# Kernel optimization log

Measured on AMD Instinct MI355X. Metric: run time of the kernel, lower is better.

Reference implementation:

```python
import jax, jax.numpy as jnp
import numpy as np

NUM_SRC = 100000  # block src nodes
NUM_DST = 50000   # block dst nodes (first NUM_DST of src in DGL convention)
E = 800000        # edges, avg in-degree 16
D = 128           # in_dim == out_dim


def setup_inputs() -> dict:
    key = jax.random.key(0)
    k0, k1, k2, k3, k4 = jax.random.split(key, 5)
    h = jax.random.normal(k0, (NUM_SRC, D), dtype=jnp.float32)
    src = jax.random.randint(k1, (E,), 0, NUM_SRC)
    dst = jax.random.randint(k2, (E,), 0, NUM_DST)
    # GraphConv params: weight (in_dim, out_dim), bias (out_dim,)
    W = jax.random.normal(k3, (D, D), dtype=jnp.float32) / np.float32(np.sqrt(D))
    b = jnp.zeros((D,), dtype=jnp.float32)
    # gene_attn: Linear(out_dim, 1, bias=False)
    w_attn = jax.random.normal(k4, (D, 1), dtype=jnp.float32) / np.float32(np.sqrt(D))
    return {"h": h, "src": src, "dst": dst, "W": W, "b": b, "w_attn": w_attn}


def reference(h, src, dst, W, b, w_attn):
    ones = jnp.ones(src.shape, dtype=h.dtype)
    # DGL GraphConv norm='both': scale by out-degree(src)^-1/2 and in-degree(dst)^-1/2,
    # degrees clamped to min 1 (allow_zero_in_degree=True).
    deg_src = jax.ops.segment_sum(ones, src, num_segments=NUM_SRC)
    deg_dst = jax.ops.segment_sum(ones, dst, num_segments=NUM_DST)
    h_src = h * jax.lax.rsqrt(jnp.maximum(deg_src, 1.0))[:, None]
    # gather neighbor feats [E, D] then scatter-sum into dst nodes
    agg = jax.ops.segment_sum(h_src[src], dst, num_segments=NUM_DST)
    agg = agg * jax.lax.rsqrt(jnp.maximum(deg_dst, 1.0))[:, None]
    # in_dim == out_dim -> aggregate-then-weight (DGL order)
    out = agg @ W + b  # h[:num_dst] equivalent: agg is already dst-sized
    alpha = jax.nn.sigmoid(out @ w_attn)  # [NUM_DST, 1]
    return out * alpha, alpha
```

## Files before the change

### kernel.cpp

```cpp
#include <hip/hip_runtime.h>
#include <hip/hip_bf16.h>
#include <math.h>

#define DD 128
#define MAXDEG 64
#define BKT 64
#define NB_MAX 1024
#define P_CH 8192
#define HBINS 16384
#define HBLK  32
#define HTHR  1024

using bf16x8 = __attribute__((ext_vector_type(8))) short;
using f32x4  = __attribute__((ext_vector_type(4))) float;

struct alignas(16) bfq { __hip_bfloat162 q[4]; };

__device__ inline float bf2f(short s) {
    unsigned int u = ((unsigned int)(unsigned short)s) << 16;
    float f;
    __builtin_memcpy(&f, &u, 4);
    return f;
}

__global__ __launch_bounds__(1024) void k1_kernel(
        const int* __restrict__ src, const int* __restrict__ dst,
        unsigned int* __restrict__ parts, unsigned int* __restrict__ bucket_cnt,
        int E, int NB, int nHist) {
    __shared__ unsigned int smem[HBINS];
    int t = threadIdx.x;
    int bid = blockIdx.x;
    if (bid < nHist) {
        int pass = bid / HBLK;
        int blk  = bid % HBLK;
        int lo   = pass * HBINS;
        for (int i = t; i < HBINS; i += 1024) smem[i] = 0;
        __syncthreads();
        int chunk = (E + HBLK - 1) / HBLK;
        int c0 = blk * chunk;
        int c1 = c0 + chunk; if (c1 > E) c1 = E;
        for (int i = c0 + t; i < c1; i += 1024) {
            unsigned int u = (unsigned int)(src[i] - lo);
            if (u < HBINS) atomicAdd(&smem[u], 1u);
        }
        __syncthreads();
        unsigned int* dstp = parts + ((size_t)bid << 14);
        for (int i = t; i < HBINS; i += 1024) dstp[i] = smem[i];
    } else {
        int b2 = bid - nHist;
        for (int b = t; b < NB; b += 1024) smem[b] = 0;
        __syncthreads();
        int c0 = b2 * P_CH;
        int c1 = c0 + P_CH; if (c1 > E) c1 = E;
        for (int i = c0 + t; i < c1; i += 1024)
            atomicAdd(&smem[dst[i] >> 6], 1u);
        __syncthreads();
        for (int b = t; b < NB; b += 1024)
            if (smem[b]) atomicAdd(&bucket_cnt[b], smem[b]);
    }
}

__global__ __launch_bounds__(256) void k2_kernel(
        const unsigned int* __restrict__ parts, unsigned int* __restrict__ deg_src,
        int num_src, const unsigned int* __restrict__ bucket_cnt,
        unsigned int* __restrict__ bucket_base, unsigned int* __restrict__ bucket_cur,
        int NB, int nMerge) {
    int bid = blockIdx.x;
    if (bid < nMerge) {
        int g = bid * 256 + threadIdx.x;
        if (g >= num_src) return;
        int pass = g >> 14;
        int r = g & (HBINS - 1);
        const unsigned int* p = parts + ((size_t)(pass * HBLK) << 14) + r;
        unsigned int s = 0;
#pragma unroll
        for (int b = 0; b < HBLK; ++b) s += p[(size_t)b << 14];
        deg_src[g] = s;
    } else {
        int lane = threadIdx.x;
        if (lane >= 64) return;
        unsigned int carry = 0;
        for (int b0 = 0; b0 < NB; b0 += 64) {
            int i = b0 + lane;
            unsigned int v = (i < NB) ? bucket_cnt[i] : 0u;
            unsigned int incl = v;
#pragma unroll
            for (int off = 1; off < 64; off <<= 1) {
                unsigned int u = __shfl_up(incl, off);
                if (lane >= off) incl += u;
            }
            unsigned int excl = incl - v + carry;
            if (i < NB) { bucket_base[i] = excl; bucket_cur[i] = excl; }
            carry += __shfl(incl, 63);
        }
        if (lane == 0) bucket_base[NB] = carry;
    }
}

__global__ __launch_bounds__(1024) void k3_kernel(
        const float* __restrict__ h, const unsigned int* __restrict__ deg_src,
        __hip_bfloat16* __restrict__ hb, const float* __restrict__ Wm,
        __hip_bfloat16* __restrict__ Wt, const int* __restrict__ src,
        const int* __restrict__ dst, unsigned int* __restrict__ bucket_cur,
        unsigned int* __restrict__ eparts, int E, int NB, int num_src,
        int nConv, int nWt) {
    __shared__ unsigned int smem[15360];
    int t = threadIdx.x;
    int bid = blockIdx.x;
    if (bid < nConv) {
        int idx = bid * 1024 + t;
        int total = num_src * (DD / 8);
        if (idx >= total) return;
        int row = idx >> 4;
        int c0  = (idx & 15) * 8;
        float nrm = rsqrtf(fmaxf((float)deg_src[row], 1.0f));
        const float4* p = reinterpret_cast<const float4*>(h + (size_t)row * DD + c0);
        float4 a = p[0], b = p[1];
        bfq o;
        o.q[0] = __float22bfloat162_rn(make_float2(a.x * nrm, a.y * nrm));
        o.q[1] = __float22bfloat162_rn(make_float2(a.z * nrm, a.w * nrm));
        o.q[2] = __float22bfloat162_rn(make_float2(b.x * nrm, b.y * nrm));
        o.q[3] = __float22bfloat162_rn(make_float2(b.z * nrm, b.w * nrm));
        *reinterpret_cast<bfq*>(hb + (size_t)row * DD + c0) = o;
    } else if (bid < nConv + nWt) {
        int idx = (bid - nConv) * 1024 + t;
        if (idx < DD * DD) {
            int c = idx >> 7, k = idx & 127;
            Wt[idx] = __float2bfloat16(Wm[k * DD + c]);
        }
    } else {
        int b2 = bid - nConv - nWt;
        unsigned int*   stage_s = smem;
        unsigned short* stage_d = (unsigned short*)(smem + 8192);
        unsigned int*   lhist   = smem + 12288;
        unsigned int*   lbase   = smem + 13312;
        unsigned int*   gbase   = smem + 14336;
        for (int b = t; b < NB_MAX; b += 1024) lhist[b] = 0;
        __syncthreads();
        int c0 = b2 * P_CH;
        int cnt = E - c0; if (cnt > P_CH) cnt = P_CH;
        int dreg[8], sreg[8];
#pragma unroll
        for (int k = 0; k < 8; ++k) {
            int j = t + k * 1024;
            if (j < cnt) {
                dreg[k] = dst[c0 + j];
                sreg[k] = src[c0 + j];
                atomicAdd(&lhist[dreg[k] >> 6], 1u);
            }
        }
        __syncthreads();
        int wid = t >> 6, lane = t & 63;
        unsigned int v = lhist[t];
        unsigned int x = v;
#pragma unroll
        for (int off = 1; off < 64; off <<= 1) {
            unsigned int u = __shfl_up(x, off);
            if (lane >= off) x += u;
        }
        if (lane == 63) gbase[wid] = x;
        __syncthreads();
        if (t < 16) {
            unsigned int w = gbase[t];
            unsigned int y = w;
#pragma unroll
            for (int off = 1; off < 16; off <<= 1) {
                unsigned int u = __shfl_up(y, off);
                if (t >= off) y += u;
            }
            gbase[t] = y - w;
        }
        __syncthreads();
        unsigned int excl = x - v + gbase[wid];
        __syncthreads();
        lbase[t] = excl;
        if (t < NB) {
            unsigned int c = lhist[t];
            gbase[t] = c ? atomicAdd(&bucket_cur[t], c) : 0u;
            lhist[t] = 0u;
        }
        __syncthreads();
#pragma unroll
        for (int k = 0; k < 8; ++k) {
            int j = t + k * 1024;
            if (j < cnt) {
                int bin = dreg[k] >> 6;
                unsigned int pos = lbase[bin] + atomicAdd(&lhist[bin], 1u);
                stage_d[pos] = (unsigned short)dreg[k];
                stage_s[pos] = (unsigned int)sreg[k];
            }
        }
        __syncthreads();
        for (int idx = t; idx < cnt; idx += 1024) {
            unsigned int d = stage_d[idx];
            unsigned int bin = d >> 6;
            unsigned int pos = gbase[bin] + ((unsigned int)idx - lbase[bin]);
            eparts[pos] = ((d & 63u) << 24) | stage_s[idx];
        }
    }
}

__global__ __launch_bounds__(512) void bgather_mfma_kernel(
        const __hip_bfloat16* __restrict__ hb,
        const unsigned int* __restrict__ eparts,
        const unsigned int* __restrict__ bucket_base,
        const __hip_bfloat16* __restrict__ Wt,
        const float* __restrict__ bias, const float* __restrict__ w_attn,
        float* __restrict__ out, float* __restrict__ alpha_out, int num_dst) {
    __shared__ unsigned int lcsr[BKT * MAXDEG];
    __shared__ unsigned int cur[BKT];
    __shared__ __hip_bfloat16 sagg[BKT * DD];
    int t = threadIdx.x, wid = t >> 6, lane = t & 63;
    int b = blockIdx.x;
    if (t < BKT) cur[t] = 0;
    __syncthreads();
    unsigned int e0 = bucket_base[b], e1 = bucket_base[b + 1];
    for (unsigned int i = e0 + t; i < e1; i += 512) {
        unsigned int e = eparts[i];
        unsigned int dlow = e >> 24;
        unsigned int pos = atomicAdd(&cur[dlow], 1u);
        if (pos < MAXDEG) lcsr[dlow * MAXDEG + pos] = e & 0xFFFFFFu;
    }
    __syncthreads();

    const bf16x8* hb8 = reinterpret_cast<const bf16x8*>(hb);
    char* sb = (char*)sagg;
    int g  = lane >> 4;
    int gl = lane & 15;
#pragma unroll
    for (int pass = 0; pass < 2; ++pass) {
        int r = pass * 32 + wid * 4 + g;
        unsigned int degu = cur[r];
        int deg = (int)degu; if (deg > MAXDEG) deg = MAXDEG;
        const unsigned int* crow = &lcsr[r * MAXDEG];
        float acc[8];
#pragma unroll
        for (int j = 0; j < 8; ++j) acc[j] = 0.f;
        int i = 0;
        for (; i + 4 <= deg; i += 4) {
            uint4 q = *reinterpret_cast<const uint4*>(crow + i);
            bf16x8 v0 = hb8[(size_t)q.x * 16 + gl];
            bf16x8 v1 = hb8[(size_t)q.y * 16 + gl];
            bf16x8 v2 = hb8[(size_t)q.z * 16 + gl];
            bf16x8 v3 = hb8[(size_t)q.w * 16 + gl];
#pragma unroll
            for (int j = 0; j < 8; ++j)
                acc[j] += (bf2f(v0[j]) + bf2f(v1[j])) + (bf2f(v2[j]) + bf2f(v3[j]));
        }
        for (; i < deg; ++i) {
            bf16x8 v = hb8[(size_t)crow[i] * 16 + gl];
#pragma unroll
            for (int j = 0; j < 8; ++j) acc[j] += bf2f(v[j]);
        }
        float scd = rsqrtf(fmaxf((float)degu, 1.0f));
        bfq o;
#pragma unroll
        for (int j = 0; j < 4; ++j)
            o.q[j] = __float22bfloat162_rn(
                make_float2(acc[2 * j] * scd, acc[2 * j + 1] * scd));
        int byte = r * 256 + gl * 16;
        *reinterpret_cast<bfq*>(sb + (byte ^ ((r & 7) << 4))) = o;
    }
    __syncthreads();

    if (wid < 4) {
        int col = lane & 15, hi = lane >> 4;
        int row0 = b * 64 + wid * 16;
        f32x4 acc[8];
#pragma unroll
        for (int ct = 0; ct < 8; ++ct) acc[ct] = (f32x4)0.f;
#pragma unroll
        for (int kg = 0; kg < 4; ++kg) {
            int arow = wid * 16 + col;
            int byte = arow * 256 + (kg * 32 + hi * 8) * 2;
            bf16x8 a = *reinterpret_cast<const bf16x8*>(
                sb + (byte ^ ((arow & 7) << 4)));
#pragma unroll
            for (int ct = 0; ct < 8; ++ct) {
                const bf16x8* B = reinterpret_cast<const bf16x8*>(
                    Wt + (size_t)(ct * 16 + col) * DD);
                bf16x8 bb = B[kg * 4 + hi];
                acc[ct] = __builtin_amdgcn_mfma_f32_16x16x32_bf16(a, bb, acc[ct],
                                                                  0, 0, 0);
            }
        }
        float wv[8], bv[8];
#pragma unroll
        for (int ct = 0; ct < 8; ++ct) {
            wv[ct] = w_attn[ct * 16 + col];
            bv[ct] = bias[ct * 16 + col];
        }
#pragma unroll
        for (int r = 0; r < 4; ++r) {
            int row = row0 + hi * 4 + r;
            float v[8];
            float s = 0.f;
#pragma unroll
            for (int ct = 0; ct < 8; ++ct) {
                v[ct] = acc[ct][r] + bv[ct];
                s = fmaf(v[ct], wv[ct], s);
            }
            s += __shfl_xor(s, 1);
            s += __shfl_xor(s, 2);
            s += __shfl_xor(s, 4);
            s += __shfl_xor(s, 8);
            float alpha = 1.0f / (1.0f + expf(-s));
            if (row < num_dst) {
#pragma unroll
                for (int ct = 0; ct < 8; ++ct)
                    out[(size_t)row * DD + ct * 16 + col] = v[ct] * alpha;
                if (col == 0) alpha_out[row] = alpha;
            }
        }
    }
}

__global__ void hist_atomic_kernel(const int* __restrict__ src,
                                   unsigned int* __restrict__ deg_src, int E) {
    int i = blockIdx.x * blockDim.x + threadIdx.x;
    if (i < E) atomicAdd(&deg_src[src[i]], 1u);
}

__global__ void fillc_kernel(const int* __restrict__ src, const int* __restrict__ dst,
                             unsigned int* __restrict__ cursor,
                             int* __restrict__ csr, int E) {
    int i = blockIdx.x * blockDim.x + threadIdx.x;
    if (i < E) {
        int s = src[i];
        int d = dst[i];
        unsigned int pos = atomicAdd(&cursor[d], 1u);
        if (pos < MAXDEG) csr[(size_t)d * MAXDEG + pos] = s;
    }
}

__global__ __launch_bounds__(256) void gather_kernel(
        const __hip_bfloat16* __restrict__ hb,
        const int* __restrict__ csr, const unsigned int* __restrict__ cursor,
        __hip_bfloat16* __restrict__ aggb, int num_dst) {
    int wave = threadIdx.x >> 6;
    int lane = threadIdx.x & 63;
    int row = blockIdx.x * 4 + wave;
    if (row >= num_dst) return;
    unsigned int degu = cursor[row];
    int deg = (int)degu; if (deg > MAXDEG) deg = MAXDEG;
    const int* crow = csr + (size_t)row * MAXDEG;
    int c = lane * 2;
    float ax = 0.f, ay = 0.f;
    int i = 0;
    for (; i + 4 <= deg; i += 4) {
        int4 s0 = *reinterpret_cast<const int4*>(crow + i);
        float2 v0 = __bfloat1622float2(*reinterpret_cast<const __hip_bfloat162*>(hb + (size_t)s0.x * DD + c));
        float2 v1 = __bfloat1622float2(*reinterpret_cast<const __hip_bfloat162*>(hb + (size_t)s0.y * DD + c));
        float2 v2 = __bfloat1622float2(*reinterpret_cast<const __hip_bfloat162*>(hb + (size_t)s0.z * DD + c));
        float2 v3 = __bfloat1622float2(*reinterpret_cast<const __hip_bfloat162*>(hb + (size_t)s0.w * DD + c));
        ax += v0.x + v1.x + v2.x + v3.x;
        ay += v0.y + v1.y + v2.y + v3.y;
    }
    for (; i < deg; ++i) {
        int s = crow[i];
        float2 vv = __bfloat1622float2(*reinterpret_cast<const __hip_bfloat162*>(hb + (size_t)s * DD + c));
        ax += vv.x; ay += vv.y;
    }
    float scd = rsqrtf(fmaxf((float)degu, 1.0f));
    *reinterpret_cast<__hip_bfloat162*>(aggb + (size_t)row * DD + c) =
        __float22bfloat162_rn(make_float2(ax * scd, ay * scd));
}

__global__ __launch_bounds__(256) void out_mfma_kernel(
        const __hip_bfloat16* __restrict__ aggb,
        const __hip_bfloat16* __restrict__ Wt,
        const float* __restrict__ bias, const float* __restrict__ w_attn,
        float* __restrict__ out, float* __restrict__ alpha_out, int num_dst) {
    int wave = threadIdx.x >> 6;
    int lane = threadIdx.x & 63;
    int row0 = blockIdx.x * 64 + wave * 16;
    if (row0 >= num_dst) return;
    int col = lane & 15;
    int hi  = lane >> 4;
    int arow = row0 + col;
    if (arow >= num_dst) arow = num_dst - 1;
    f32x4 acc[8];
#pragma unroll
    for (int ct = 0; ct < 8; ++ct) acc[ct] = (f32x4)0.f;
    const bf16x8* A = reinterpret_cast<const bf16x8*>(aggb + (size_t)arow * DD);
#pragma unroll
    for (int kg = 0; kg < 4; ++kg) {
        bf16x8 a = A[kg * 4 + hi];
#pragma unroll
        for (int ct = 0; ct < 8; ++ct) {
            const bf16x8* B =
                reinterpret_cast<const bf16x8*>(Wt + (size_t)(ct * 16 + col) * DD);
            bf16x8 b = B[kg * 4 + hi];
            acc[ct] = __builtin_amdgcn_mfma_f32_16x16x32_bf16(a, b, acc[ct], 0, 0, 0);
        }
    }
    float wv[8], bv[8];
#pragma unroll
    for (int ct = 0; ct < 8; ++ct) {
        wv[ct] = w_attn[ct * 16 + col];
        bv[ct] = bias[ct * 16 + col];
    }
#pragma unroll
    for (int r = 0; r < 4; ++r) {
        int row = row0 + hi * 4 + r;
        float v[8];
        float s = 0.f;
#pragma unroll
        for (int ct = 0; ct < 8; ++ct) {
            v[ct] = acc[ct][r] + bv[ct];
            s = fmaf(v[ct], wv[ct], s);
        }
        s += __shfl_xor(s, 1);
        s += __shfl_xor(s, 2);
        s += __shfl_xor(s, 4);
        s += __shfl_xor(s, 8);
        float alpha = 1.0f / (1.0f + expf(-s));
        if (row < num_dst) {
#pragma unroll
            for (int ct = 0; ct < 8; ++ct)
                out[(size_t)row * DD + ct * 16 + col] = v[ct] * alpha;
            if (col == 0) alpha_out[row] = alpha;
        }
    }
}

extern "C" void kernel_launch(void* const* d_in, const int* in_sizes, int n_in,
                              void* d_out, int out_size, void* d_ws, size_t ws_size,
                              hipStream_t stream) {
    const float* h      = (const float*)d_in[0];
    const int*   src    = (const int*)d_in[1];
    const int*   dst    = (const int*)d_in[2];
    const float* Wm     = (const float*)d_in[3];
    const float* bias   = (const float*)d_in[4];
    const float* w_attn = (const float*)d_in[5];

    int num_src = in_sizes[0] / DD;
    int E       = in_sizes[1];
    int num_dst = out_size / (DD + 1);
    int NB      = (num_dst + BKT - 1) / BKT;
    int NPASS   = (num_src + HBINS - 1) / HBINS;

    float* out       = (float*)d_out;
    float* alpha_out = out + (size_t)num_dst * DD;

    char* p = (char*)d_ws;
    auto take = [&p](size_t bytes) {
        char* q = p;
        p += (bytes + 255) & ~(size_t)255;
        return q;
    };
    unsigned int* deg_src = (unsigned int*)take((size_t)num_src * 4);
    unsigned int* cursor  = (unsigned int*)take((size_t)num_dst * 4);
    int*          csr     = (int*)take((size_t)num_dst * MAXDEG * 4);
    __hip_bfloat16* aggb  = (__hip_bfloat16*)take((size_t)num_dst * DD * 2);
    __hip_bfloat16* Wt    = (__hip_bfloat16*)take((size_t)DD * DD * 2);
    __hip_bfloat16* hb    = (__hip_bfloat16*)take((size_t)num_src * DD * 2);
    unsigned int* parts   = (unsigned int*)take(((size_t)NPASS * HBLK) << 16);
    size_t full_need = (size_t)(p - (char*)d_ws);

    unsigned int* eparts      = (unsigned int*)csr;
    unsigned int* bucket_cnt  = eparts + ((E + 7) & ~7);
    unsigned int* bucket_base = bucket_cnt + NB + 8;
    unsigned int* bucket_cur  = bucket_base + NB + 8;

    bool use_mp = ws_size >= full_need;
    bool bucket_ok = use_mp && NB <= NB_MAX && num_dst <= 65536 &&
                     num_src < (1 << 24) &&
                     ((size_t)E + 3 * NB + 32) * 4 <= (size_t)num_dst * MAXDEG * 4;

    int thr = 256;
    int nHist  = NPASS * HBLK;
    int nPc    = (E + P_CH - 1) / P_CH;
    int nMerge = (num_src + 255) / 256;
    int nConv  = (num_src * (DD / 8) + 1023) / 1024;
    int nWt    = (DD * DD + 1023) / 1024;

    if (bucket_ok) {
        hipMemsetAsync(bucket_cnt, 0, (size_t)NB * 4, stream);
        k1_kernel<<<nHist + nPc, 1024, 0, stream>>>(src, dst, parts, bucket_cnt,
                                                    E, NB, nHist);
        k2_kernel<<<nMerge + 1, 256, 0, stream>>>(parts, deg_src, num_src,
                                                  bucket_cnt, bucket_base,
                                                  bucket_cur, NB, nMerge);
        k3_kernel<<<nConv + nWt + nPc, 1024, 0, stream>>>(
            h, deg_src, hb, Wm, Wt, src, dst, bucket_cur, eparts, E, NB, num_src,
            nConv, nWt);
        bgather_mfma_kernel<<<NB, 512, 0, stream>>>(hb, eparts, bucket_base, Wt,
                                                    bias, w_attn, out, alpha_out,
                                                    num_dst);
    } else if (use_mp) {
        hipMemsetAsync(cursor, 0, (size_t)num_dst * 4, stream);
        k1_kernel<<<nHist, 1024, 0, stream>>>(src, dst, parts, cursor ,
                                              E, 0, nHist);
        k2_kernel<<<nMerge, 256, 0, stream>>>(parts, deg_src, num_src, cursor,
                                              cursor, cursor, 0, nMerge);
        fillc_kernel<<<(E + thr - 1) / thr, thr, 0, stream>>>(src, dst, cursor,
                                                              csr, E);
        k3_kernel<<<nConv + nWt, 1024, 0, stream>>>(
            h, deg_src, hb, Wm, Wt, src, dst, cursor, (unsigned int*)csr, E, 0,
            num_src, nConv, nWt);
        int grid_g = (num_dst + 3) / 4;
        gather_kernel<<<grid_g, thr, 0, stream>>>(hb, csr, cursor, aggb, num_dst);
        int grid_c = (num_dst + 63) / 64;
        out_mfma_kernel<<<grid_c, thr, 0, stream>>>(aggb, Wt, bias, w_attn,
                                                    out, alpha_out, num_dst);
    } else {
        hipMemsetAsync(deg_src, 0, (size_t)num_src * 4, stream);
        hipMemsetAsync(cursor, 0, (size_t)num_dst * 4, stream);
        hist_atomic_kernel<<<(E + thr - 1) / thr, thr, 0, stream>>>(src, deg_src, E);
        fillc_kernel<<<(E + thr - 1) / thr, thr, 0, stream>>>(src, dst, cursor,
                                                              csr, E);
        k3_kernel<<<nConv + nWt, 1024, 0, stream>>>(
            h, deg_src, hb, Wm, Wt, src, dst, cursor, (unsigned int*)csr, E, 0,
            num_src, nConv, nWt);
        int grid_g = (num_dst + 3) / 4;
        gather_kernel<<<grid_g, thr, 0, stream>>>(hb, csr, cursor, aggb, num_dst);
        int grid_c = (num_dst + 63) / 64;
        out_mfma_kernel<<<grid_c, thr, 0, stream>>>(aggb, Wt, bias, w_attn,
                                                    out, alpha_out, num_dst);
    }
}
```

Baseline: 103.4 us.

## Split each 64-node bucket across four 256-thread blocks and deepen gather unroll

The fused gather+MFMA kernel now launches four blocks per 64-destination bucket. Each block scans the whole bucket edge list but keeps only edges for its 16 destinations, gathers in a single pass, and runs one MFMA wave. This raises the block count and shrinks per-block LDS, which should improve occupancy and load balance on the many CUs. The cost is reading each bucket's edge list four times. Separately, an 8-wide unrolled gather loop is added to keep more independent loads in flight.

```diff
diff --git a/kernel.cpp b/kernel.cpp
--- a/kernel.cpp
+++ b/kernel.cpp
@@ -5,6 +5,7 @@
 #define DD 128
 #define MAXDEG 64
 #define BKT 64
+#define SBKT 16
 #define NB_MAX 1024
 #define P_CH 8192
 #define HBINS 16384
@@ -200,26 +201,29 @@
     }
 }
 
-__global__ __launch_bounds__(512) void bgather_mfma_kernel(
+__global__ __launch_bounds__(256) void bgather_mfma_kernel(
         const __hip_bfloat16* __restrict__ hb,
         const unsigned int* __restrict__ eparts,
         const unsigned int* __restrict__ bucket_base,
         const __hip_bfloat16* __restrict__ Wt,
         const float* __restrict__ bias, const float* __restrict__ w_attn,
         float* __restrict__ out, float* __restrict__ alpha_out, int num_dst) {
-    __shared__ unsigned int lcsr[BKT * MAXDEG];
-    __shared__ unsigned int cur[BKT];
-    __shared__ __hip_bfloat16 sagg[BKT * DD];
+    __shared__ unsigned int lcsr[SBKT * MAXDEG];
+    __shared__ unsigned int cur[SBKT];
+    __shared__ __hip_bfloat16 sagg[SBKT * DD];
     int t = threadIdx.x, wid = t >> 6, lane = t & 63;
-    int b = blockIdx.x;
-    if (t < BKT) cur[t] = 0;
+    int b = blockIdx.x >> 2;
+    unsigned int quarter = blockIdx.x & 3;
+    if (t < SBKT) cur[t] = 0;
     __syncthreads();
     unsigned int e0 = bucket_base[b], e1 = bucket_base[b + 1];
-    for (unsigned int i = e0 + t; i < e1; i += 512) {
+    for (unsigned int i = e0 + t; i < e1; i += 256) {
         unsigned int e = eparts[i];
         unsigned int dlow = e >> 24;
-        unsigned int pos = atomicAdd(&cur[dlow], 1u);
-        if (pos < MAXDEG) lcsr[dlow * MAXDEG + pos] = e & 0xFFFFFFu;
+        if ((dlow >> 4) == quarter) {
+            unsigned int pos = atomicAdd(&cur[dlow & 15], 1u);
+            if (pos < MAXDEG) lcsr[(dlow & 15) * MAXDEG + pos] = e & 0xFFFFFFu;
+        }
     }
     __syncthreads();
 
@@ -227,9 +231,8 @@
     char* sb = (char*)sagg;
     int g  = lane >> 4;
     int gl = lane & 15;
-#pragma unroll
-    for (int pass = 0; pass < 2; ++pass) {
-        int r = pass * 32 + wid * 4 + g;
+    {
+        int r = wid * 4 + g;
         unsigned int degu = cur[r];
         int deg = (int)degu; if (deg > MAXDEG) deg = MAXDEG;
         const unsigned int* crow = &lcsr[r * MAXDEG];
@@ -237,6 +240,22 @@
 #pragma unroll
         for (int j = 0; j < 8; ++j) acc[j] = 0.f;
         int i = 0;
+        for (; i + 8 <= deg; i += 8) {
+            uint4 qa = *reinterpret_cast<const uint4*>(crow + i);
+            uint4 qb = *reinterpret_cast<const uint4*>(crow + i + 4);
+            bf16x8 v0 = hb8[(size_t)qa.x * 16 + gl];
+            bf16x8 v1 = hb8[(size_t)qa.y * 16 + gl];
+            bf16x8 v2 = hb8[(size_t)qa.z * 16 + gl];
+            bf16x8 v3 = hb8[(size_t)qa.w * 16 + gl];
+            bf16x8 v4 = hb8[(size_t)qb.x * 16 + gl];
+            bf16x8 v5 = hb8[(size_t)qb.y * 16 + gl];
+            bf16x8 v6 = hb8[(size_t)qb.z * 16 + gl];
+            bf16x8 v7 = hb8[(size_t)qb.w * 16 + gl];
+#pragma unroll
+            for (int j = 0; j < 8; ++j)
+                acc[j] += ((bf2f(v0[j]) + bf2f(v1[j])) + (bf2f(v2[j]) + bf2f(v3[j])))
+                        + ((bf2f(v4[j]) + bf2f(v5[j])) + (bf2f(v6[j]) + bf2f(v7[j])));
+        }
         for (; i + 4 <= deg; i += 4) {
             uint4 q = *reinterpret_cast<const uint4*>(crow + i);
             bf16x8 v0 = hb8[(size_t)q.x * 16 + gl];
@@ -263,18 +282,17 @@
     }
     __syncthreads();
 
-    if (wid < 4) {
+    if (wid == 0) {
         int col = lane & 15, hi = lane >> 4;
-        int row0 = b * 64 + wid * 16;
+        int row0 = b * 64 + quarter * 16;
         f32x4 acc[8];
 #pragma unroll
         for (int ct = 0; ct < 8; ++ct) acc[ct] = (f32x4)0.f;
 #pragma unroll
         for (int kg = 0; kg < 4; ++kg) {
-            int arow = wid * 16 + col;
-            int byte = arow * 256 + (kg * 32 + hi * 8) * 2;
+            int byte = col * 256 + (kg * 32 + hi * 8) * 2;
             bf16x8 a = *reinterpret_cast<const bf16x8*>(
-                sb + (byte ^ ((arow & 7) << 4)));
+                sb + (byte ^ ((col & 7) << 4)));
 #pragma unroll
             for (int ct = 0; ct < 8; ++ct) {
                 const bf16x8* B = reinterpret_cast<const bf16x8*>(
@@ -485,9 +503,9 @@
         k3_kernel<<<nConv + nWt + nPc, 1024, 0, stream>>>(
             h, deg_src, hb, Wm, Wt, src, dst, bucket_cur, eparts, E, NB, num_src,
             nConv, nWt);
-        bgather_mfma_kernel<<<NB, 512, 0, stream>>>(hb, eparts, bucket_base, Wt,
-                                                    bias, w_attn, out, alpha_out,
-                                                    num_dst);
+        bgather_mfma_kernel<<<NB * 4, 256, 0, stream>>>(hb, eparts, bucket_base, Wt,
+                                                        bias, w_attn, out, alpha_out,
+                                                        num_dst);
     } else if (use_mp) {
         hipMemsetAsync(cursor, 0, (size_t)num_dst * 4, stream);
         k1_kernel<<<nHist, 1024, 0, stream>>>(src, dst, parts, cursor ,
```

After: 95.25 us (median of 2 runs). 1.09x faster.
